# Kernel optimization log

Measured on AMD Instinct MI355X. Metric: run time of the kernel, lower is better.

## Reference

```python
import jax, jax.numpy as jnp
import numpy as np

N, C, H, W = 32, 256, 64, 64
K = 1024  # embed_size


def setup_inputs() -> dict:
    key = jax.random.key(0)
    k1, k2 = jax.random.split(key)
    x = jax.random.normal(k1, (N, C, H, W), dtype=jnp.float32)
    embed = jax.random.normal(k2, (K, C), dtype=jnp.float32)  # codebook buffer
    return {"x": x, "embed": embed}


def reference(x, embed):
    n, c, h, w = x.shape
    # [N,C,H,W] -> [N*H*W, C]
    flat = jnp.transpose(x, (0, 2, 3, 1)).reshape(-1, c)
    # squared euclidean distance; sqrt omitted since argmin is invariant
    d = (
        jnp.sum(flat * flat, axis=-1, keepdims=True)
        - 2.0 * flat @ embed.T
        + jnp.sum(embed * embed, axis=-1)
    )  # [N*H*W, K]
    embed_idx = jnp.argmin(d, axis=1).reshape(n, h, w)
    quantize = embed[embed_idx]  # [N,H,W,C]
    quantize = jnp.transpose(quantize, (0, 3, 1, 2))  # [N,C,H,W]
    diff = jnp.mean((jax.lax.stop_gradient(quantize) - x) ** 2)
    quantize = x + jax.lax.stop_gradient(quantize - x)  # straight-through
    return quantize, embed_idx, diff
```

## Files before the change

kernel.cpp:

```cpp
#include <hip/hip_runtime.h>

#define NB    32
#define CDIM  256
#define HWSZ  4096
#define NPOS  (NB*HWSZ)
#define KCODES 1024
#define QELEMS ((size_t)NB*CDIM*HWSZ)
#define IDX_OFF QELEMS
#define DIFF_OFF (QELEMS + NPOS)
#define E2F_OFF 393216

typedef _Float16       f16x8  __attribute__((ext_vector_type(8)));
typedef float          f32x4  __attribute__((ext_vector_type(4)));
typedef unsigned short u16x8  __attribute__((ext_vector_type(8)));

static __device__ inline unsigned short f2h(float f) {
    _Float16 h = (_Float16)f;
    return __builtin_bit_cast(unsigned short, h);
}

__global__ __launch_bounds__(64) void vq_prep_embed(const float* __restrict__ embed,
                                                    float* __restrict__ out) {
    const int k = blockIdx.x;
    const int lane = threadIdx.x;
    const float4 v = *reinterpret_cast<const float4*>(embed + (size_t)k * CDIM + lane * 4);

    unsigned char* __restrict__ ebuf = (unsigned char*)out;

    _Float16 h0 = (_Float16)v.x, h1 = (_Float16)v.y, h2 = (_Float16)v.z, h3 = (_Float16)v.w;
    ushort4 hv = { __builtin_bit_cast(unsigned short, h0), __builtin_bit_cast(unsigned short, h1),
                   __builtin_bit_cast(unsigned short, h2), __builtin_bit_cast(unsigned short, h3) };
    ushort4 lv = { f2h((v.x - (float)h0) * 2048.0f), f2h((v.y - (float)h1) * 2048.0f),
                   f2h((v.z - (float)h2) * 2048.0f), f2h((v.w - (float)h3) * 2048.0f) };

    const int cc = k >> 8;
    const int cr = k & 255;
    const int sw = cr & 7;
    auto put = [&](int kp, ushort4 val) {
        const int kq = kp >> 6, off = kp & 63, slot = off >> 3, sub = off & 7;
        const size_t byte = (size_t)(cc * 12 + kq) * 32768 + (size_t)cr * 128
                          + (size_t)(((slot ^ sw) << 4) + sub * 2);
        *reinterpret_cast<ushort4*>(ebuf + byte) = val;
    };
    put(lane * 4, hv);
    put(256 + lane * 4, lv);
    put(512 + lane * 4, hv);

    float s = v.x * v.x + v.y * v.y + v.z * v.z + v.w * v.w;
    #pragma unroll
    for (int m = 1; m < 64; m <<= 1) s += __shfl_xor(s, m, 64);
    if (lane == 0) out[E2F_OFF + k] = s;
    if (k == 0 && lane == 0) out[DIFF_OFF] = 0.0f;
}

#define ABYTES 65536
#define BBYTES 32768
#define B0OFF  ABYTES
#define SCROFF (ABYTES + 2*BBYTES)

__global__ __launch_bounds__(512, 2) void vq_stage1(const float* __restrict__ x,
                                                    float* __restrict__ out) {
    __shared__ __align__(16) unsigned char lds[SCROFF + 2048];

    const unsigned char* __restrict__ ebuf = (const unsigned char*)out;
    const float* __restrict__ e2buf = out + E2F_OFF;
    float* __restrict__ idx_out = out + IDX_OFF;

    const int t    = threadIdx.x;
    const int lane = t & 63;
    const int col  = lane & 15;
    const int kgrp = lane >> 4;
    const int widx = t >> 6;
    const int wy   = widx >> 2;
    const int wx   = widx & 3;

    const int pos0 = blockIdx.x * 64;
    const int n    = pos0 >> 12;
    const int hw0  = pos0 & 4095;
    const float* __restrict__ xbase = x + (size_t)n * (CDIM * HWSZ) + hw0;

    {
        const int i = t & 63;
        const int g = t >> 6;
        unsigned char* arow = lds + i * 1024;
        const int sw = (i & 7) << 4;
        float x2p = 0.f;
        #pragma unroll
        for (int it = 0; it < 4; ++it) {
            const int cb = g * 32 + it * 8;
            u16x8 hv, lv;
            #pragma unroll
            for (int j = 0; j < 8; ++j) {
                float vv = xbase[(size_t)(cb + j) * HWSZ + i];
                x2p = fmaf(vv, vv, x2p);
                _Float16 hh = (_Float16)vv;
                hv[j] = __builtin_bit_cast(unsigned short, hh);
                lv[j] = f2h((vv - (float)hh) * 2048.0f);
            }
            *reinterpret_cast<u16x8*>(arow + ((cb * 2) ^ sw))       = hv;
            *reinterpret_cast<u16x8*>(arow + ((512 + cb * 2) ^ sw)) = lv;
        }
        ((float*)(lds + SCROFF))[g * 64 + i] = x2p;
    }

    auto stage = [&](int tile, int buf) {
        const unsigned char* src = ebuf + (size_t)tile * BBYTES;
        unsigned char* dst = lds + B0OFF + buf * BBYTES;
        #pragma unroll
        for (int ii = 0; ii < 4; ++ii) {
            const int chunk = (widx * 4 + ii) * 1024;
            __builtin_amdgcn_global_load_lds(
                (const __attribute__((address_space(1))) unsigned int*)(src + chunk + lane * 16),
                (__attribute__((address_space(3))) unsigned int*)(dst + chunk),
                16, 0, 0);
        }
    };

    stage(0, 0);

    float e2pre[16];
    #pragma unroll
    for (int cc = 0; cc < 4; ++cc)
        #pragma unroll
        for (int cf = 0; cf < 4; ++cf)
            e2pre[cc * 4 + cf] = e2buf[cc * 256 + wx * 64 + cf * 16 + col];

    __syncthreads();

    float x2r[8];
    {
        const float* x2p = (const float*)(lds + SCROFF);
        #pragma unroll
        for (int rg = 0; rg < 2; ++rg)
            #pragma unroll
            for (int reg = 0; reg < 4; ++reg) {
                const int row = wy * 32 + rg * 16 + kgrp * 4 + reg;
                float s = 0.f;
                #pragma unroll
                for (int g = 0; g < 8; ++g) s += x2p[g * 64 + row];
                x2r[rg * 4 + reg] = s;
            }
    }

    float bestv[8];
    int   besti[8];
    #pragma unroll
    for (int sl = 0; sl < 8; ++sl) { bestv[sl] = 3.4e38f; besti[sl] = 0; }

    const f32x4 zero4 = {0.f, 0.f, 0.f, 0.f};
    int cur = 0, tile = 0;

    for (int cc = 0; cc < 4; ++cc) {
        f32x4 accA[2][4], accB[2][4];
        #pragma unroll
        for (int rg = 0; rg < 2; ++rg)
            #pragma unroll
            for (int cf = 0; cf < 4; ++cf) { accA[rg][cf] = zero4; accB[rg][cf] = zero4; }

        for (int kq = 0; kq < 12; ++kq, ++tile) {
            if (tile + 1 < 48) stage(tile + 1, cur ^ 1);

            const unsigned char* bbase = lds + B0OFF + cur * BBYTES;
            const int mbase = (kq < 4) ? kq * 64 : kq * 64 - 256;

            __builtin_amdgcn_s_setprio(1);
            #pragma unroll
            for (int kk = 0; kk < 2; ++kk) {
                f16x8 a[2], b[4];
                #pragma unroll
                for (int rg = 0; rg < 2; ++rg) {
                    const int row = wy * 32 + rg * 16 + col;
                    const int byte = row * 1024 + ((mbase + kk * 32 + kgrp * 8) << 1);
                    a[rg] = *reinterpret_cast<const f16x8*>(lds + (byte ^ ((row & 7) << 4)));
                }
                #pragma unroll
                for (int cf = 0; cf < 4; ++cf) {
                    const int brow = wx * 64 + cf * 16 + col;
                    const int byte = brow * 128 + kk * 64 + kgrp * 16;
                    b[cf] = *reinterpret_cast<const f16x8*>(bbase + (byte ^ ((brow & 7) << 4)));
                }
                if (kq < 4) {
                    #pragma unroll
                    for (int rg = 0; rg < 2; ++rg)
                        #pragma unroll
                        for (int cf = 0; cf < 4; ++cf)
                            accA[rg][cf] = __builtin_amdgcn_mfma_f32_16x16x32_f16(
                                a[rg], b[cf], accA[rg][cf], 0, 0, 0);
                } else {
                    #pragma unroll
                    for (int rg = 0; rg < 2; ++rg)
                        #pragma unroll
                        for (int cf = 0; cf < 4; ++cf)
                            accB[rg][cf] = __builtin_amdgcn_mfma_f32_16x16x32_f16(
                                a[rg], b[cf], accB[rg][cf], 0, 0, 0);
                }
            }
            __builtin_amdgcn_s_setprio(0);

            __syncthreads();
            cur ^= 1;
        }

        #pragma unroll
        for (int cf = 0; cf < 4; ++cf) {
            const int code = cc * 256 + wx * 64 + cf * 16 + col;
            const float ec = e2pre[cc * 4 + cf];
            #pragma unroll
            for (int rg = 0; rg < 2; ++rg)
                #pragma unroll
                for (int reg = 0; reg < 4; ++reg) {
                    const float dot = accA[rg][cf][reg] + accB[rg][cf][reg] * (1.0f / 2048.0f);
                    const float s = (x2r[rg * 4 + reg] - 2.0f * dot) + ec;
                    const int sl = rg * 4 + reg;
                    if (s < bestv[sl]) { bestv[sl] = s; besti[sl] = code; }
                }
        }
    }

    #pragma unroll
    for (int sl = 0; sl < 8; ++sl) {
        #pragma unroll
        for (int m = 1; m < 16; m <<= 1) {
            float ov = __shfl_xor(bestv[sl], m, 64);
            int   oi = __shfl_xor(besti[sl], m, 64);
            if (ov < bestv[sl] || (ov == bestv[sl] && oi < besti[sl])) {
                bestv[sl] = ov; besti[sl] = oi;
            }
        }
    }

    {
        float* mv = (float*)(lds + SCROFF);
        int*   mi = (int*)(lds + SCROFF + 1024);
        if (wx != 0 && col == 0) {
            #pragma unroll
            for (int rg = 0; rg < 2; ++rg)
                #pragma unroll
                for (int reg = 0; reg < 4; ++reg) {
                    const int p = wy * 32 + rg * 16 + kgrp * 4 + reg;
                    mv[(wx - 1) * 64 + p] = bestv[rg * 4 + reg];
                    mi[(wx - 1) * 64 + p] = besti[rg * 4 + reg];
                }
        }
        __syncthreads();
        if (wx == 0 && col == 0) {
            float dsum = 0.f;
            #pragma unroll
            for (int rg = 0; rg < 2; ++rg)
                #pragma unroll
                for (int reg = 0; reg < 4; ++reg) {
                    const int sl = rg * 4 + reg;
                    const int p = wy * 32 + rg * 16 + kgrp * 4 + reg;
                    #pragma unroll
                    for (int w = 0; w < 3; ++w) {
                        const float ov = mv[w * 64 + p];
                        const int   oi = mi[w * 64 + p];
                        if (ov < bestv[sl] || (ov == bestv[sl] && oi < besti[sl])) {
                            bestv[sl] = ov; besti[sl] = oi;
                        }
                    }
                    idx_out[pos0 + p] = (float)besti[sl];
                    dsum += bestv[sl];
                }
            atomicAdd(out + DIFF_OFF, dsum * (1.0f / 33554432.0f));
        }
    }
}

__global__ __launch_bounds__(256) void vq_gather_kernel(const float* __restrict__ embed,
                                                        float* __restrict__ out) {
    const int tid = threadIdx.x;
    const int p = blockIdx.x * 256 + tid;
    const int n = p >> 12;
    const int hw = p & 4095;
    const int idx = (int)out[IDX_OFF + p];
    const float4* __restrict__ erow4 = reinterpret_cast<const float4*>(embed + (size_t)idx * CDIM);
    float* __restrict__ op = out + (size_t)n * (CDIM * HWSZ) + hw;

    #pragma unroll 8
    for (int c4 = 0; c4 < 64; ++c4) {
        const float4 e = erow4[c4];
        op[(size_t)(c4 * 4 + 0) * HWSZ] = e.x;
        op[(size_t)(c4 * 4 + 1) * HWSZ] = e.y;
        op[(size_t)(c4 * 4 + 2) * HWSZ] = e.z;
        op[(size_t)(c4 * 4 + 3) * HWSZ] = e.w;
    }
}

extern "C" void kernel_launch(void* const* d_in, const int* in_sizes, int n_in,
                              void* d_out, int out_size, void* d_ws, size_t ws_size,
                              hipStream_t stream) {
    const float* x = (const float*)d_in[0];
    const float* embed = (const float*)d_in[1];
    float* out = (float*)d_out;

    vq_prep_embed<<<KCODES, 64, 0, stream>>>(embed, out);
    vq_stage1<<<NPOS / 64, 512, 0, stream>>>(x, out);
    vq_gather_kernel<<<NPOS / 256, 256, 0, stream>>>(embed, out);
}
```

Before: 362.4 us.

## Switch VQ distance GEMM to 32x32x16 MFMA with full-codebook accumulators per wave

```diff
diff --git a/kernel.cpp b/kernel.cpp
--- a/kernel.cpp
+++ b/kernel.cpp
@@ -8,10 +8,19 @@
 #define QELEMS ((size_t)NB*CDIM*HWSZ)
 #define IDX_OFF QELEMS
 #define DIFF_OFF (QELEMS + NPOS)
-#define E2F_OFF 393216
+#define EBYTES (32*32768)
+#define E2F_OFF (EBYTES/4)
+
+#define AOFF  0
+#define BOFF  65536
+#define X2P   131072
+#define X2T   133120
+#define MVOFF 133376
+#define MIOFF 135424
+#define LDSSZ 137472
 
 typedef _Float16       f16x8  __attribute__((ext_vector_type(8)));
-typedef float          f32x4  __attribute__((ext_vector_type(4)));
+typedef float          f32x16 __attribute__((ext_vector_type(16)));
 typedef unsigned short u16x8  __attribute__((ext_vector_type(8)));
 
 static __device__ inline unsigned short f2h(float f) {
@@ -30,21 +39,16 @@
     _Float16 h0 = (_Float16)v.x, h1 = (_Float16)v.y, h2 = (_Float16)v.z, h3 = (_Float16)v.w;
     ushort4 hv = { __builtin_bit_cast(unsigned short, h0), __builtin_bit_cast(unsigned short, h1),
                    __builtin_bit_cast(unsigned short, h2), __builtin_bit_cast(unsigned short, h3) };
-    ushort4 lv = { f2h((v.x - (float)h0) * 2048.0f), f2h((v.y - (float)h1) * 2048.0f),
-                   f2h((v.z - (float)h2) * 2048.0f), f2h((v.w - (float)h3) * 2048.0f) };
-
-    const int cc = k >> 8;
-    const int cr = k & 255;
-    const int sw = cr & 7;
-    auto put = [&](int kp, ushort4 val) {
-        const int kq = kp >> 6, off = kp & 63, slot = off >> 3, sub = off & 7;
-        const size_t byte = (size_t)(cc * 12 + kq) * 32768 + (size_t)cr * 128
-                          + (size_t)(((slot ^ sw) << 4) + sub * 2);
-        *reinterpret_cast<ushort4*>(ebuf + byte) = val;
-    };
-    put(lane * 4, hv);
-    put(256 + lane * 4, lv);
-    put(512 + lane * 4, hv);
+    ushort4 lv = { f2h((v.x - (float)h0) * 64.0f), f2h((v.y - (float)h1) * 64.0f),
+                   f2h((v.z - (float)h2) * 64.0f), f2h((v.w - (float)h3) * 64.0f) };
+
+    const int c0   = lane * 4;
+    const int tile = c0 >> 4;
+    const int kh   = (c0 >> 3) & 1;
+    const int sub  = c0 & 7;
+    const size_t byte = (size_t)tile * 32768 + (size_t)kh * 16384 + (size_t)k * 16 + sub * 2;
+    *reinterpret_cast<ushort4*>(ebuf + byte)              = hv;
+    *reinterpret_cast<ushort4*>(ebuf + byte + 16 * 32768) = lv;
 
     float s = v.x * v.x + v.y * v.y + v.z * v.z + v.w * v.w;
     #pragma unroll
@@ -53,26 +57,19 @@
     if (k == 0 && lane == 0) out[DIFF_OFF] = 0.0f;
 }
 
-#define ABYTES 65536
-#define BBYTES 32768
-#define B0OFF  ABYTES
-#define SCROFF (ABYTES + 2*BBYTES)
-
 __global__ __launch_bounds__(512, 2) void vq_stage1(const float* __restrict__ x,
                                                     float* __restrict__ out) {
-    __shared__ __align__(16) unsigned char lds[SCROFF + 2048];
+    __shared__ __align__(16) unsigned char lds[LDSSZ];
 
     const unsigned char* __restrict__ ebuf = (const unsigned char*)out;
     const float* __restrict__ e2buf = out + E2F_OFF;
     float* __restrict__ idx_out = out + IDX_OFF;
 
-    const int t    = threadIdx.x;
-    const int lane = t & 63;
-    const int col  = lane & 15;
-    const int kgrp = lane >> 4;
-    const int widx = t >> 6;
-    const int wy   = widx >> 2;
-    const int wx   = widx & 3;
+    const int t     = threadIdx.x;
+    const int lane  = t & 63;
+    const int col32 = lane & 31;
+    const int hi    = lane >> 5;
+    const int widx  = t >> 6;
 
     const int pos0 = blockIdx.x * 64;
     const int n    = pos0 >> 12;
@@ -82,30 +79,31 @@
     {
         const int i = t & 63;
         const int g = t >> 6;
-        unsigned char* arow = lds + i * 1024;
-        const int sw = (i & 7) << 4;
         float x2p = 0.f;
         #pragma unroll
-        for (int it = 0; it < 4; ++it) {
-            const int cb = g * 32 + it * 8;
+        for (int j = 0; j < 4; ++j) {
+            const int c0 = g * 32 + j * 8;
             u16x8 hv, lv;
             #pragma unroll
-            for (int j = 0; j < 8; ++j) {
-                float vv = xbase[(size_t)(cb + j) * HWSZ + i];
+            for (int q = 0; q < 8; ++q) {
+                float vv = xbase[(size_t)(c0 + q) * HWSZ + i];
                 x2p = fmaf(vv, vv, x2p);
                 _Float16 hh = (_Float16)vv;
-                hv[j] = __builtin_bit_cast(unsigned short, hh);
-                lv[j] = f2h((vv - (float)hh) * 2048.0f);
-            }
-            *reinterpret_cast<u16x8*>(arow + ((cb * 2) ^ sw))       = hv;
-            *reinterpret_cast<u16x8*>(arow + ((512 + cb * 2) ^ sw)) = lv;
-        }
-        ((float*)(lds + SCROFF))[g * 64 + i] = x2p;
+                hv[q] = __builtin_bit_cast(unsigned short, hh);
+                lv[q] = f2h((vv - (float)hh) * 64.0f);
+            }
+            const int a  = c0 >> 4;
+            const int kh = (c0 >> 3) & 1;
+            const int byte = a * 2048 + kh * 1024 + i * 16;
+            *reinterpret_cast<u16x8*>(lds + byte)         = hv;
+            *reinterpret_cast<u16x8*>(lds + byte + 32768) = lv;
+        }
+        ((float*)(lds + X2P))[g * 64 + i] = x2p;
     }
 
     auto stage = [&](int tile, int buf) {
-        const unsigned char* src = ebuf + (size_t)tile * BBYTES;
-        unsigned char* dst = lds + B0OFF + buf * BBYTES;
+        const unsigned char* src = ebuf + (size_t)tile * 32768;
+        unsigned char* dst = lds + BOFF + buf * 32768;
         #pragma unroll
         for (int ii = 0; ii < 4; ++ii) {
             const int chunk = (widx * 4 + ii) * 1024;
@@ -117,153 +115,116 @@
     };
 
     stage(0, 0);
-
-    float e2pre[16];
-    #pragma unroll
-    for (int cc = 0; cc < 4; ++cc)
-        #pragma unroll
-        for (int cf = 0; cf < 4; ++cf)
-            e2pre[cc * 4 + cf] = e2buf[cc * 256 + wx * 64 + cf * 16 + col];
-
     __syncthreads();
 
-    float x2r[8];
-    {
-        const float* x2p = (const float*)(lds + SCROFF);
-        #pragma unroll
-        for (int rg = 0; rg < 2; ++rg)
-            #pragma unroll
-            for (int reg = 0; reg < 4; ++reg) {
-                const int row = wy * 32 + rg * 16 + kgrp * 4 + reg;
-                float s = 0.f;
-                #pragma unroll
-                for (int g = 0; g < 8; ++g) s += x2p[g * 64 + row];
-                x2r[rg * 4 + reg] = s;
-            }
-    }
-
-    float bestv[8];
-    int   besti[8];
-    #pragma unroll
-    for (int sl = 0; sl < 8; ++sl) { bestv[sl] = 3.4e38f; besti[sl] = 0; }
-
-    const f32x4 zero4 = {0.f, 0.f, 0.f, 0.f};
-    int cur = 0, tile = 0;
-
-    for (int cc = 0; cc < 4; ++cc) {
-        f32x4 accA[2][4], accB[2][4];
-        #pragma unroll
-        for (int rg = 0; rg < 2; ++rg)
-            #pragma unroll
-            for (int cf = 0; cf < 4; ++cf) { accA[rg][cf] = zero4; accB[rg][cf] = zero4; }
-
-        for (int kq = 0; kq < 12; ++kq, ++tile) {
-            if (tile + 1 < 48) stage(tile + 1, cur ^ 1);
-
-            const unsigned char* bbase = lds + B0OFF + cur * BBYTES;
-            const int mbase = (kq < 4) ? kq * 64 : kq * 64 - 256;
-
-            __builtin_amdgcn_s_setprio(1);
-            #pragma unroll
-            for (int kk = 0; kk < 2; ++kk) {
-                f16x8 a[2], b[4];
-                #pragma unroll
-                for (int rg = 0; rg < 2; ++rg) {
-                    const int row = wy * 32 + rg * 16 + col;
-                    const int byte = row * 1024 + ((mbase + kk * 32 + kgrp * 8) << 1);
-                    a[rg] = *reinterpret_cast<const f16x8*>(lds + (byte ^ ((row & 7) << 4)));
-                }
-                #pragma unroll
-                for (int cf = 0; cf < 4; ++cf) {
-                    const int brow = wx * 64 + cf * 16 + col;
-                    const int byte = brow * 128 + kk * 64 + kgrp * 16;
-                    b[cf] = *reinterpret_cast<const f16x8*>(bbase + (byte ^ ((brow & 7) << 4)));
-                }
-                if (kq < 4) {
-                    #pragma unroll
-                    for (int rg = 0; rg < 2; ++rg)
-                        #pragma unroll
-                        for (int cf = 0; cf < 4; ++cf)
-                            accA[rg][cf] = __builtin_amdgcn_mfma_f32_16x16x32_f16(
-                                a[rg], b[cf], accA[rg][cf], 0, 0, 0);
-                } else {
-                    #pragma unroll
-                    for (int rg = 0; rg < 2; ++rg)
-                        #pragma unroll
-                        for (int cf = 0; cf < 4; ++cf)
-                            accB[rg][cf] = __builtin_amdgcn_mfma_f32_16x16x32_f16(
-                                a[rg], b[cf], accB[rg][cf], 0, 0, 0);
-                }
-            }
-            __builtin_amdgcn_s_setprio(0);
-
-            __syncthreads();
-            cur ^= 1;
-        }
-
-        #pragma unroll
-        for (int cf = 0; cf < 4; ++cf) {
-            const int code = cc * 256 + wx * 64 + cf * 16 + col;
-            const float ec = e2pre[cc * 4 + cf];
-            #pragma unroll
-            for (int rg = 0; rg < 2; ++rg)
-                #pragma unroll
-                for (int reg = 0; reg < 4; ++reg) {
-                    const float dot = accA[rg][cf][reg] + accB[rg][cf][reg] * (1.0f / 2048.0f);
-                    const float s = (x2r[rg * 4 + reg] - 2.0f * dot) + ec;
-                    const int sl = rg * 4 + reg;
-                    if (s < bestv[sl]) { bestv[sl] = s; besti[sl] = code; }
-                }
-        }
-    }
-
-    #pragma unroll
-    for (int sl = 0; sl < 8; ++sl) {
-        #pragma unroll
-        for (int m = 1; m < 16; m <<= 1) {
-            float ov = __shfl_xor(bestv[sl], m, 64);
-            int   oi = __shfl_xor(besti[sl], m, 64);
-            if (ov < bestv[sl] || (ov == bestv[sl] && oi < besti[sl])) {
-                bestv[sl] = ov; besti[sl] = oi;
-            }
-        }
-    }
-
-    {
-        float* mv = (float*)(lds + SCROFF);
-        int*   mi = (int*)(lds + SCROFF + 1024);
-        if (wx != 0 && col == 0) {
-            #pragma unroll
-            for (int rg = 0; rg < 2; ++rg)
-                #pragma unroll
-                for (int reg = 0; reg < 4; ++reg) {
-                    const int p = wy * 32 + rg * 16 + kgrp * 4 + reg;
-                    mv[(wx - 1) * 64 + p] = bestv[rg * 4 + reg];
-                    mi[(wx - 1) * 64 + p] = besti[rg * 4 + reg];
-                }
-        }
+    if (t < 64) {
+        const float* p = (const float*)(lds + X2P);
+        float s = 0.f;
+        #pragma unroll
+        for (int g = 0; g < 8; ++g) s += p[g * 64 + t];
+        ((float*)(lds + X2T))[t] = s;
+    }
+
+    f32x16 acc[2][4];
+    #pragma unroll
+    for (int ra = 0; ra < 2; ++ra)
+        #pragma unroll
+        for (int cb = 0; cb < 4; ++cb)
+            #pragma unroll
+            for (int r = 0; r < 16; ++r) acc[ra][cb][r] = 0.f;
+
+    const int aoff_lane = hi * 1024 + col32 * 16;
+    const int boff_lane = hi * 16384 + (widx * 128 + col32) * 16;
+
+    int buf = 0;
+    for (int kq = 0; kq < 48; ++kq) {
+        const int nb = kq + 1;
+        if (nb < 48) stage(nb < 32 ? nb : nb - 32, buf ^ 1);
+
+        const int a = (kq < 16) ? kq : kq - 16;
+        const unsigned char* ab = lds + a * 2048;
+        const unsigned char* bb = lds + BOFF + buf * 32768;
+
+        f16x8 av[2], bv[4];
+        #pragma unroll
+        for (int ra = 0; ra < 2; ++ra)
+            av[ra] = *reinterpret_cast<const f16x8*>(ab + aoff_lane + ra * 512);
+        #pragma unroll
+        for (int cb = 0; cb < 4; ++cb)
+            bv[cb] = *reinterpret_cast<const f16x8*>(bb + boff_lane + cb * 512);
+
+        if (kq >= 16 && kq < 32) {
+            #pragma unroll
+            for (int ra = 0; ra < 2; ++ra) av[ra] *= (_Float16)0.015625f;
+        } else if (kq >= 32) {
+            #pragma unroll
+            for (int cb = 0; cb < 4; ++cb) bv[cb] *= (_Float16)0.015625f;
+        }
+
+        __builtin_amdgcn_s_setprio(1);
+        #pragma unroll
+        for (int ra = 0; ra < 2; ++ra)
+            #pragma unroll
+            for (int cb = 0; cb < 4; ++cb)
+                acc[ra][cb] = __builtin_amdgcn_mfma_f32_32x32x16_f16(
+                    av[ra], bv[cb], acc[ra][cb], 0, 0, 0);
+        __builtin_amdgcn_s_setprio(0);
+
         __syncthreads();
-        if (wx == 0 && col == 0) {
-            float dsum = 0.f;
-            #pragma unroll
-            for (int rg = 0; rg < 2; ++rg)
-                #pragma unroll
-                for (int reg = 0; reg < 4; ++reg) {
-                    const int sl = rg * 4 + reg;
-                    const int p = wy * 32 + rg * 16 + kgrp * 4 + reg;
-                    #pragma unroll
-                    for (int w = 0; w < 3; ++w) {
-                        const float ov = mv[w * 64 + p];
-                        const int   oi = mi[w * 64 + p];
-                        if (ov < bestv[sl] || (ov == bestv[sl] && oi < besti[sl])) {
-                            bestv[sl] = ov; besti[sl] = oi;
-                        }
-                    }
-                    idx_out[pos0 + p] = (float)besti[sl];
-                    dsum += bestv[sl];
-                }
-            atomicAdd(out + DIFF_OFF, dsum * (1.0f / 33554432.0f));
-        }
+        buf ^= 1;
+    }
+
+    const float* x2t = (const float*)(lds + X2T);
+    float e2v[4];
+    #pragma unroll
+    for (int cb = 0; cb < 4; ++cb)
+        e2v[cb] = e2buf[widx * 128 + cb * 32 + col32];
+
+    float* mv = (float*)(lds + MVOFF);
+    int*   mi = (int*)(lds + MIOFF);
+
+    #pragma unroll
+    for (int ra = 0; ra < 2; ++ra) {
+        #pragma unroll
+        for (int reg = 0; reg < 16; ++reg) {
+            const int pos = ra * 32 + (reg & 3) + 8 * (reg >> 2) + 4 * hi;
+            const float x2 = x2t[pos];
+            float bv_ = 3.4e38f;
+            int   bi_ = 0;
+            #pragma unroll
+            for (int cb = 0; cb < 4; ++cb) {
+                const int code = widx * 128 + cb * 32 + col32;
+                const float s = (x2 - 2.0f * acc[ra][cb][reg]) + e2v[cb];
+                if (s < bv_) { bv_ = s; bi_ = code; }
+            }
+            #pragma unroll
+            for (int m = 1; m < 32; m <<= 1) {
+                float ov = __shfl_xor(bv_, m, 64);
+                int   oi = __shfl_xor(bi_, m, 64);
+                if (ov < bv_ || (ov == bv_ && oi < bi_)) { bv_ = ov; bi_ = oi; }
+            }
+            if (col32 == 0) {
+                mv[widx * 64 + pos] = bv_;
+                mi[widx * 64 + pos] = bi_;
+            }
+        }
+    }
+
+    __syncthreads();
+    if (t < 64) {
+        float bv_ = mv[t];
+        int   bi_ = mi[t];
+        #pragma unroll
+        for (int w = 1; w < 8; ++w) {
+            const float ov = mv[w * 64 + t];
+            const int   oi = mi[w * 64 + t];
+            if (ov < bv_ || (ov == bv_ && oi < bi_)) { bv_ = ov; bi_ = oi; }
+        }
+        idx_out[pos0 + t] = (float)bi_;
+        float d = bv_;
+        #pragma unroll
+        for (int m = 1; m < 64; m <<= 1) d += __shfl_xor(d, m, 64);
+        if (t == 0) atomicAdd(out + DIFF_OFF, d * (1.0f / 33554432.0f));
     }
 }
 
```

Measured after the change: 431.9 us. 1.19x slower.
